# Kernel tuning notes

Measured on AMD Instinct MI355X. Metric: run time of the kernel, lower is better.

Reference implementation:

```python
import jax, jax.numpy as jnp
import numpy as np

EPS = 1e-6
H, KV, HD, FF = 16, 8, 128, 3072

def rmsnorm(x, scale):
    # qwen3_compatible: compute in fp32, scale, cast back
    xf = x.astype(jnp.float32)
    var = jnp.mean(xf * xf, axis=-1, keepdims=True)
    return ((xf * jax.lax.rsqrt(var + EPS)) * scale).astype(x.dtype)

def apply_rope(x, cos, sin):
    # x: [b, h, s, d]; cos/sin: [s, d]
    d = x.shape[-1]
    x1, x2 = x[..., : d // 2], x[..., d // 2 :]
    rotated = jnp.concatenate([-x2, x1], axis=-1)
    return (x * cos[None, None] + rotated * sin[None, None]).astype(x.dtype)

def setup_inputs() -> dict:
    key = jax.random.key(0)
    B, S, D = 2, 2048, 1024
    ks = jax.random.split(key, 8)
    x = jax.random.normal(ks[0], (B, S, D), jnp.float32)
    mask = jnp.triu(jnp.ones((S, S), dtype=bool), k=1)  # True = masked (causal)
    # Qwen3 RoPE, base 1e6, full-dim cos/sin (halves duplicated)
    pos = jnp.arange(S, dtype=jnp.float32)
    inv_freq = 1.0 / (1e6 ** (jnp.arange(0, HD, 2, dtype=jnp.float32) / HD))
    ang = pos[:, None] * inv_freq[None, :]
    cos = jnp.concatenate([jnp.cos(ang), jnp.cos(ang)], axis=-1)
    sin = jnp.concatenate([jnp.sin(ang), jnp.sin(ang)], axis=-1)
    s = 0.02
    wq = jax.random.normal(ks[1], (D, H * HD), jnp.float32) * s
    wk = jax.random.normal(ks[2], (D, KV * HD), jnp.float32) * s
    wv = jax.random.normal(ks[3], (D, KV * HD), jnp.float32) * s
    wo = jax.random.normal(ks[4], (H * HD, D), jnp.float32) * s
    fc1 = jax.random.normal(ks[5], (D, FF), jnp.float32) * s
    fc2 = jax.random.normal(ks[6], (D, FF), jnp.float32) * s
    fc3 = jax.random.normal(ks[7], (FF, D), jnp.float32) * s
    return dict(x=x, mask=mask, cos=cos, sin=sin, wq=wq, wk=wk, wv=wv, wo=wo,
                fc1=fc1, fc2=fc2, fc3=fc3,
                norm1_scale=jnp.ones((D,), jnp.float32),
                norm2_scale=jnp.ones((D,), jnp.float32),
                q_norm_scale=jnp.ones((HD,), jnp.float32),
                k_norm_scale=jnp.ones((HD,), jnp.float32))

def reference(x, mask, cos, sin, wq, wk, wv, wo, fc1, fc2, fc3,
              norm1_scale, norm2_scale, q_norm_scale, k_norm_scale):
    B, S, D = x.shape
    G = H // KV  # GQA group size
    # --- attention sublayer ---
    h = rmsnorm(x, norm1_scale)
    q = (h @ wq).reshape(B, S, H, HD).transpose(0, 2, 1, 3)   # [b,h,s,d]
    k = (h @ wk).reshape(B, S, KV, HD).transpose(0, 2, 1, 3)  # [b,kv,s,d]
    v = (h @ wv).reshape(B, S, KV, HD).transpose(0, 2, 1, 3)
    q = rmsnorm(q, q_norm_scale)
    k = rmsnorm(k, k_norm_scale)
    q = apply_rope(q, cos, sin)
    k = apply_rope(k, cos, sin)
    k = jnp.repeat(k, G, axis=1)  # repeat_interleave over head dim
    v = jnp.repeat(v, G, axis=1)
    scores = jnp.einsum('bhqd,bhkd->bhqk', q, k)
    scores = jnp.where(mask[None, None], -jnp.inf, scores)
    w = jax.nn.softmax(scores / np.float32(np.sqrt(HD)), axis=-1)
    ctx = jnp.einsum('bhqk,bhkd->bqhd', w, v).reshape(B, S, H * HD)
    x = x + ctx @ wo
    # --- SwiGLU FFN sublayer ---
    h2 = rmsnorm(x, norm2_scale)
    ff = (jax.nn.silu(h2 @ fc1) * (h2 @ fc2)) @ fc3
    return x + ff
```

## Files before the change

kernel.cpp:

```cpp
#include <hip/hip_runtime.h>

#define B_  2
#define S_  2048
#define D_  1024
#define H_  16
#define KV_ 8
#define HD_ 128
#define FF_ 3072
#define KVB 32

typedef short bf16x8 __attribute__((ext_vector_type(8)));
typedef short bf16x4 __attribute__((ext_vector_type(4)));
typedef float f32x4 __attribute__((ext_vector_type(4)));

__device__ __forceinline__ float bf2f(unsigned short u) {
    union { float f; unsigned int i; } c; c.i = ((unsigned int)u) << 16; return c.f;
}
__device__ __forceinline__ unsigned short f2bf(float f) {
    union { float f; unsigned int i; } c; c.f = f;
    unsigned int r = c.i + 0x7fffu + ((c.i >> 16) & 1u);
    return (unsigned short)(r >> 16);
}

__device__ __forceinline__ void gload_lds16(const unsigned short* g, char* ldsbase) {
    __builtin_amdgcn_global_load_lds(
        (const __attribute__((address_space(1))) unsigned int*)g,
        (__attribute__((address_space(3))) unsigned int*)ldsbase, 16, 0, 0);
}

__device__ __forceinline__ f32x4 pv_mfma(bf16x4 a, bf16x4 b, f32x4 c) {
#if __has_builtin(__builtin_amdgcn_mfma_f32_16x16x16bf16_1k)
    return __builtin_amdgcn_mfma_f32_16x16x16bf16_1k(a, b, c, 0, 0, 0);
#elif __has_builtin(__builtin_amdgcn_mfma_f32_16x16x16_bf16)
    return __builtin_amdgcn_mfma_f32_16x16x16_bf16(a, b, c, 0, 0, 0);
#else
    f32x4 d;
    asm("v_mfma_f32_16x16x16_bf16 %0, %1, %2, %3" : "=v"(d) : "v"(a), "v"(b), "v"(c));
    return d;
#endif
}

__global__ __launch_bounds__(256)
void rmsnorm_kernel(const float* __restrict__ in, const float* __restrict__ scale,
                    unsigned short* __restrict__ out) {
    const int row = blockIdx.x;
    const int t = threadIdx.x;
    const float4 v = *reinterpret_cast<const float4*>(in + (size_t)row * D_ + t * 4);
    float s = v.x * v.x + v.y * v.y + v.z * v.z + v.w * v.w;
    #pragma unroll
    for (int o = 32; o; o >>= 1) s += __shfl_down(s, o);
    __shared__ float red[4];
    const int lane = t & 63, wid = t >> 6;
    if (lane == 0) red[wid] = s;
    __syncthreads();
    s = red[0] + red[1] + red[2] + red[3];
    const float rn = rsqrtf(s * (1.0f / D_) + 1e-6f);
    const float4 sc = *reinterpret_cast<const float4*>(scale + t * 4);
    unsigned short o4[4];
    o4[0] = f2bf(v.x * rn * sc.x);
    o4[1] = f2bf(v.y * rn * sc.y);
    o4[2] = f2bf(v.z * rn * sc.z);
    o4[3] = f2bf(v.w * rn * sc.w);
    *reinterpret_cast<ushort4*>(out + (size_t)row * D_ + t * 4) =
        *reinterpret_cast<ushort4*>(o4);
}

__global__ __launch_bounds__(256)
void wtrans_kernel(const float* __restrict__ W, unsigned short* __restrict__ Wt,
                   int K, int N) {
    __shared__ float tile[32][33];
    const int t = threadIdx.x;
    const int kt = blockIdx.x * 32, nt = blockIdx.y * 32;
    {
        const int r = t >> 3, c4 = (t & 7) * 4;
        const float4 v = *reinterpret_cast<const float4*>(W + (size_t)(kt + r) * N + nt + c4);
        tile[r][c4] = v.x; tile[r][c4 + 1] = v.y; tile[r][c4 + 2] = v.z; tile[r][c4 + 3] = v.w;
    }
    __syncthreads();
    {
        const int n = t >> 3, k4 = (t & 7) * 4;
        unsigned short o[4];
        #pragma unroll
        for (int i = 0; i < 4; i++) o[i] = f2bf(tile[k4 + i][n]);
        *reinterpret_cast<ushort4*>(Wt + (size_t)(nt + n) * K + kt + k4) =
            *reinterpret_cast<ushort4*>(o);
    }
}

__global__ __launch_bounds__(512, 2)
void gemm256(const unsigned short* __restrict__ A, const unsigned short* __restrict__ Bt,
             unsigned short* __restrict__ C, int M, int N, int K, int nm) {
    __shared__ __align__(16) char lds[131072];
    const int tid = threadIdx.x;
    const int lane = tid & 63, w = tid >> 6;
    const int lm = lane & 15, lg = lane >> 4;
    const int wr = w >> 2, wc = w & 3;
    const int nwg = gridDim.x;
    const int cpx = nwg >> 3;
    const int bid = blockIdx.x;
    const int swz = (bid & 7) * cpx + (bid >> 3);
    const int m0 = (swz % nm) * 256;
    const int n0 = (swz / nm) * 256;

    f32x4 acc[8][4];
    #pragma unroll
    for (int i = 0; i < 8; ++i)
        #pragma unroll
        for (int j = 0; j < 4; ++j) acc[i][j] = (f32x4){0.f, 0.f, 0.f, 0.f};

    const int srow = tid >> 3;
    const int skel = ((tid & 7) * 8) ^ (((tid >> 5) & 1) << 4);
    const int flip = ((lm >> 2) & 1) << 5;
    const int abase = (wr * 128 + lm) * 128 + ((lg * 16) ^ flip);
    const int bbase = (wc * 64 + lm) * 128 + ((lg * 16) ^ flip);

    auto part1 = [&](int kt, int d) {
        const unsigned short* ga = A + (size_t)(m0 + srow) * K + kt * 64 + skel;
        const unsigned short* gb = Bt + (size_t)(n0 + srow) * K + kt * 64 + skel;
        char* la = lds + d * 65536 + (w << 10);
        char* lb = la + 32768;
        gload_lds16(gb,                      lb);
        gload_lds16(gb + (size_t)64 * K,     lb + 8192);
        gload_lds16(gb + (size_t)128 * K,    lb + 16384);
        gload_lds16(gb + (size_t)192 * K,    lb + 24576);
        gload_lds16(ga,                      la);
        gload_lds16(ga + (size_t)128 * K,    la + 16384);
    };
    auto part2 = [&](int kt, int d) {
        const unsigned short* ga = A + (size_t)(m0 + srow) * K + kt * 64 + skel;
        char* la = lds + d * 65536 + (w << 10);
        gload_lds16(ga + (size_t)64 * K,     la + 8192);
        gload_lds16(ga + (size_t)192 * K,    la + 24576);
    };

    part1(0, 0);
    part2(0, 0);
    asm volatile("s_waitcnt vmcnt(0)" ::: "memory");
    __builtin_amdgcn_s_barrier();

    const int ntile = K >> 6;
    for (int kt = 0; kt < ntile; ++kt) {
        const int d = kt & 1;
        const bool pf = (kt + 1 < ntile);
        const char* Ar = lds + d * 65536;
        const char* Br = Ar + 32768;
        bf16x8 bb[4][2];
        #pragma unroll
        for (int nf = 0; nf < 4; ++nf)
            #pragma unroll
            for (int s = 0; s < 2; ++s)
                bb[nf][s] = *reinterpret_cast<const bf16x8*>(Br + bbase + nf * 2048 + s * 64);
        bf16x8 aH[4][2];
        #pragma unroll
        for (int f = 0; f < 4; ++f)
            #pragma unroll
            for (int s = 0; s < 2; ++s)
                aH[f][s] = *reinterpret_cast<const bf16x8*>(Ar + abase + f * 2048 + s * 64);
        if (pf) part1(kt + 1, d ^ 1);
        __builtin_amdgcn_s_setprio(1);
        #pragma unroll
        for (int f = 0; f < 4; ++f)
            #pragma unroll
            for (int nf = 0; nf < 4; ++nf)
                #pragma unroll
                for (int s = 0; s < 2; ++s)
                    acc[f][nf] = __builtin_amdgcn_mfma_f32_16x16x32_bf16(
                        aH[f][s], bb[nf][s], acc[f][nf], 0, 0, 0);
        __builtin_amdgcn_s_setprio(0);
        if (pf) asm volatile("s_waitcnt vmcnt(6)" ::: "memory");
        else    asm volatile("s_waitcnt vmcnt(0)" ::: "memory");
        __builtin_amdgcn_s_barrier();
        #pragma unroll
        for (int f = 0; f < 4; ++f)
            #pragma unroll
            for (int s = 0; s < 2; ++s)
                aH[f][s] = *reinterpret_cast<const bf16x8*>(Ar + abase + 8192 + f * 2048 + s * 64);
        if (pf) part2(kt + 1, d ^ 1);
        __builtin_amdgcn_s_setprio(1);
        #pragma unroll
        for (int f = 0; f < 4; ++f)
            #pragma unroll
            for (int nf = 0; nf < 4; ++nf)
                #pragma unroll
                for (int s = 0; s < 2; ++s)
                    acc[4 + f][nf] = __builtin_amdgcn_mfma_f32_16x16x32_bf16(
                        aH[f][s], bb[nf][s], acc[4 + f][nf], 0, 0, 0);
        __builtin_amdgcn_s_setprio(0);
        if (pf) {
            asm volatile("s_waitcnt vmcnt(2)" ::: "memory");
            __builtin_amdgcn_s_barrier();
        }
    }

    #pragma unroll
    for (int mf = 0; mf < 8; ++mf)
        #pragma unroll
        for (int nf = 0; nf < 4; ++nf)
            #pragma unroll
            for (int r = 0; r < 4; ++r)
                C[(size_t)(m0 + wr * 128 + mf * 16 + lg * 4 + r) * N +
                  (n0 + wc * 64 + nf * 16 + lm)] = f2bf(acc[mf][nf][r]);
}

template<int EPI>
__global__ __launch_bounds__(256)
void gemm_bt(const unsigned short* __restrict__ A, const unsigned short* __restrict__ Bt,
             void* __restrict__ Cout, const float* __restrict__ resid,
             int M, int N, int K, int lda) {
    constexpr int SMB = (EPI == 2) ? 34816 : 16384;
    __shared__ __align__(16) char sm[SMB];
    const int t = threadIdx.x;
    const int lane = t & 63, w = t >> 6;
    const int m0 = blockIdx.x * 128, n0 = blockIdx.y * 128;
    const int wr = w >> 1, wc = w & 1;
    const int lm = lane & 15, lg = lane >> 4;

    f32x4 acc[4][4];
    #pragma unroll
    for (int i = 0; i < 4; i++)
        #pragma unroll
        for (int j = 0; j < 4; j++) acc[i][j] = (f32x4){0.f, 0.f, 0.f, 0.f};

    const int row0 = t >> 2, kseg = (t & 3) * 8;
    const unsigned short* Ab = A + (size_t)(m0 + row0) * lda + kseg;
    const unsigned short* Bb = Bt + (size_t)(n0 + row0) * K + kseg;
    const size_t rstepA = (size_t)64 * lda;
    const size_t rstepB = (size_t)64 * K;
    char* ldsA = sm + w * 1024;
    char* ldsB = sm + 8192 + w * 1024;

    for (int k0 = 0; k0 < K; k0 += 32) {
        gload_lds16(Ab + k0, ldsA);
        gload_lds16(Ab + rstepA + k0, ldsA + 4096);
        gload_lds16(Bb + k0, ldsB);
        gload_lds16(Bb + rstepB + k0, ldsB + 4096);
        __syncthreads();
        bf16x8 aF[4], bF[4];
        #pragma unroll
        for (int i = 0; i < 4; i++)
            aF[i] = *reinterpret_cast<const bf16x8*>(sm + (wr * 64 + i * 16 + lm) * 64 + lg * 16);
        #pragma unroll
        for (int j = 0; j < 4; j++)
            bF[j] = *reinterpret_cast<const bf16x8*>(sm + 8192 + (wc * 64 + j * 16 + lm) * 64 + lg * 16);
        #pragma unroll
        for (int i = 0; i < 4; i++)
            #pragma unroll
            for (int j = 0; j < 4; j++)
                acc[i][j] = __builtin_amdgcn_mfma_f32_16x16x32_bf16(aF[i], bF[j], acc[i][j], 0, 0, 0);
        __syncthreads();
    }

    if (EPI == 2) {
        unsigned short (*Ct)[136] = reinterpret_cast<unsigned short(*)[136]>(sm);
        #pragma unroll
        for (int i = 0; i < 4; i++)
            #pragma unroll
            for (int j = 0; j < 4; j++)
                #pragma unroll
                for (int r = 0; r < 4; r++)
                    Ct[wc * 64 + j * 16 + lm][wr * 64 + i * 16 + lg * 4 + r] = f2bf(acc[i][j][r]);
        __syncthreads();
        const int colr = t >> 1, seg = t & 1;
        unsigned short* dst = reinterpret_cast<unsigned short*>(Cout) +
                              (size_t)(n0 + colr) * M + m0 + seg * 64;
        const unsigned short* srcp = &Ct[colr][seg * 64];
        #pragma unroll
        for (int i = 0; i < 8; i++)
            reinterpret_cast<uint4*>(dst)[i] = reinterpret_cast<const uint4*>(srcp)[i];
        return;
    }

    #pragma unroll
    for (int i = 0; i < 4; i++) {
        #pragma unroll
        for (int j = 0; j < 4; j++) {
            #pragma unroll
            for (int r = 0; r < 4; r++) {
                const int row = m0 + wr * 64 + i * 16 + lg * 4 + r;
                const int col = n0 + wc * 64 + j * 16 + lm;
                const size_t idx = (size_t)row * N + col;
                if (EPI == 0) {
                    reinterpret_cast<unsigned short*>(Cout)[idx] = f2bf(acc[i][j][r]);
                } else {
                    reinterpret_cast<float*>(Cout)[idx] = resid[idx] + acc[i][j][r];
                }
            }
        }
    }
}

__global__ __launch_bounds__(128)
void qknorm_rope_kernel(unsigned short* __restrict__ qk, const float* __restrict__ scale,
                        const float* __restrict__ cosb, const float* __restrict__ sinb,
                        int ld) {
    const int row = blockIdx.x;
    const int head = blockIdx.y;
    const int s = row & (S_ - 1);
    const int t = threadIdx.x;
    unsigned short* p = qk + (size_t)row * ld + head * HD_;
    const float v = bf2f(p[t]);
    float ss = v * v;
    #pragma unroll
    for (int o = 32; o; o >>= 1) ss += __shfl_down(ss, o);
    __shared__ float red[2];
    __shared__ float vals[HD_];
    const int lane = t & 63, wid = t >> 6;
    if (lane == 0) red[wid] = ss;
    __syncthreads();
    ss = red[0] + red[1];
    const float rn = rsqrtf(ss * (1.0f / HD_) + 1e-6f);
    const float nv = v * rn * scale[t];
    vals[t] = nv;
    __syncthreads();
    const float rot = (t < 64) ? -vals[t + 64] : vals[t - 64];
    const float c = cosb[(size_t)s * HD_ + t];
    const float sn = sinb[(size_t)s * HD_ + t];
    p[t] = f2bf(nv * c + rot * sn);
}

__global__ __launch_bounds__(256)
void fattn_kernel(const unsigned short* __restrict__ qg,
                  const unsigned short* __restrict__ kg,
                  const unsigned short* __restrict__ vtg,
                  unsigned short* __restrict__ out, int qld, int kld) {
    __shared__ __align__(16) char klds[2 * 8192];
    __shared__ __align__(16) char vtlds[2 * 9216];
    const int t = threadIdx.x;
    const int lane = t & 63, w = t >> 6;
    const int lm = lane & 15, lg = lane >> 4;
    const int g = blockIdx.x;
    const int h = g & 15, b = g >> 4;
    const int qt = (int)gridDim.y - 1 - (int)blockIdx.y;
    const int kvh = h >> 1;
    const int q0b = qt * 64;
    const int q0w = q0b + w * 16;
    const float CS = 0.12752409731504826f;

    const unsigned short* qbase = qg + (size_t)(b * S_ + q0w + lm) * qld + h * HD_;
    bf16x8 qf[4];
    #pragma unroll
    for (int kk = 0; kk < 4; ++kk)
        qf[kk] = *reinterpret_cast<const bf16x8*>(qbase + kk * 32 + lg * 8);

    f32x4 acc[8];
    #pragma unroll
    for (int i = 0; i < 8; ++i) acc[i] = (f32x4){0.f, 0.f, 0.f, 0.f};
    float m = -3e38f, l = 0.f;

    const int nt = 2 * qt + 2;
    const int skv = t >> 3, sd8 = t & 7;
    const int vd = t >> 1, vseg = t & 1;
    const unsigned short* kgb = kg + (size_t)b * S_ * kld + kvh * HD_;
    const unsigned short* vgb = vtg + (size_t)(kvh * HD_) * (B_ * S_) + (size_t)b * S_;

    uint4 kr0, kr1, vr0, vr1;
    auto LOADR = [&](int kt) {
        const int kv0 = kt * KVB;
        const unsigned short* ksrc = kgb + (size_t)(kv0 + skv) * kld + sd8 * 16;
        kr0 = *reinterpret_cast<const uint4*>(ksrc);
        kr1 = *reinterpret_cast<const uint4*>(ksrc + 8);
        const unsigned short* vsrc = vgb + (size_t)vd * (B_ * S_) + kv0 + vseg * 16;
        vr0 = *reinterpret_cast<const uint4*>(vsrc);
        vr1 = *reinterpret_cast<const uint4*>(vsrc + 8);
    };
    auto WRITELDS = [&](int bufi) {
        char* kd = klds + bufi * 8192 + skv * 256;
        const int sw = (skv & 7) << 4;
        *reinterpret_cast<uint4*>(kd + ((sd8 * 32) ^ sw)) = kr0;
        *reinterpret_cast<uint4*>(kd + ((sd8 * 32 + 16) ^ sw)) = kr1;
        char* vdst = vtlds + bufi * 9216 + vd * 72 + vseg * 32;
        *reinterpret_cast<uint2*>(vdst)      = make_uint2(vr0.x, vr0.y);
        *reinterpret_cast<uint2*>(vdst + 8)  = make_uint2(vr0.z, vr0.w);
        *reinterpret_cast<uint2*>(vdst + 16) = make_uint2(vr1.x, vr1.y);
        *reinterpret_cast<uint2*>(vdst + 24) = make_uint2(vr1.z, vr1.w);
    };

    LOADR(0);
    WRITELDS(0);
    __syncthreads();

    for (int kt = 0; kt < nt; ++kt) {
        const int kv0 = kt * KVB;
        const int bufi = kt & 1;
        const bool havenext = (kt + 1 < nt);
        if (havenext) LOADR(kt + 1);
        if (kv0 <= q0w + 15) {
            f32x4 st[2];
            st[0] = (f32x4){0.f, 0.f, 0.f, 0.f};
            st[1] = (f32x4){0.f, 0.f, 0.f, 0.f};
            #pragma unroll
            for (int sub = 0; sub < 2; ++sub) {
                const int kvl = sub * 16 + lm;
                const char* krow = klds + bufi * 8192 + kvl * 256;
                const int sw = (kvl & 7) << 4;
                #pragma unroll
                for (int kk = 0; kk < 4; ++kk) {
                    const bf16x8 kf = *reinterpret_cast<const bf16x8*>(krow + ((kk * 64 + lg * 16) ^ sw));
                    st[sub] = __builtin_amdgcn_mfma_f32_16x16x32_bf16(kf, qf[kk], st[sub], 0, 0, 0);
                }
            }
            if (kv0 + KVB - 1 > q0w) {
                const int qa = q0w + lm;
                #pragma unroll
                for (int sub = 0; sub < 2; ++sub)
                    #pragma unroll
                    for (int r = 0; r < 4; ++r)
                        if (kv0 + sub * 16 + lg * 4 + r > qa) st[sub][r] = -3e38f;
            }
            float pmax = st[0][0];
            #pragma unroll
            for (int r = 1; r < 4; ++r) pmax = fmaxf(pmax, st[0][r]);
            #pragma unroll
            for (int r = 0; r < 4; ++r) pmax = fmaxf(pmax, st[1][r]);
            pmax = fmaxf(pmax, __shfl_xor(pmax, 16));
            pmax = fmaxf(pmax, __shfl_xor(pmax, 32));
            if (__any(pmax - m > 8.0f)) {
                const float mn = fmaxf(pmax, m);
                const float corr = exp2f((m - mn) * CS);
                l *= corr;
                #pragma unroll
                for (int i = 0; i < 8; ++i) acc[i] *= corr;
                m = mn;
            }
            float ps = 0.f;
            bf16x4 pb[2];
            #pragma unroll
            for (int sub = 0; sub < 2; ++sub)
                #pragma unroll
                for (int r = 0; r < 4; ++r) {
                    const float pv = exp2f((st[sub][r] - m) * CS);
                    ps += pv;
                    pb[sub][r] = (short)f2bf(pv);
                }
            ps += __shfl_xor(ps, 16);
            ps += __shfl_xor(ps, 32);
            l += ps;
            #pragma unroll
            for (int sub = 0; sub < 2; ++sub) {
                const char* vb2 = vtlds + bufi * 9216 + sub * 32 + lg * 8;
                #pragma unroll
                for (int db = 0; db < 8; ++db) {
                    const bf16x4 vf = *reinterpret_cast<const bf16x4*>(vb2 + (db * 16 + lm) * 72);
                    acc[db] = pv_mfma(vf, pb[sub], acc[db]);
                }
            }
        }
        if (havenext) WRITELDS((kt + 1) & 1);
        __syncthreads();
    }
    const float inv = 1.0f / l;
    unsigned short* ob = out + (size_t)(b * S_ + q0w + lm) * qld + h * HD_ + lg * 4;
    #pragma unroll
    for (int db = 0; db < 8; ++db) {
        unsigned short r4[4];
        #pragma unroll
        for (int r = 0; r < 4; ++r) r4[r] = f2bf(acc[db][r] * inv);
        *reinterpret_cast<uint2*>(ob + db * 16) = *reinterpret_cast<uint2*>(r4);
    }
}

__global__ __launch_bounds__(256)
void silu_mul_kernel(unsigned short* __restrict__ g, int n4) {
    const int i = blockIdx.x * 256 + threadIdx.x;
    if (i >= n4) return;
    const int r = i / (FF_ / 4);
    const int c = (i - r * (FF_ / 4)) * 4;
    const size_t off = (size_t)r * (2 * FF_) + c;
    const uint2 a = *reinterpret_cast<const uint2*>(g + off);
    const uint2 bv = *reinterpret_cast<const uint2*>(g + off + FF_);
    const unsigned int au[2] = {a.x, a.y}, bu[2] = {bv.x, bv.y};
    unsigned int rr[2];
    #pragma unroll
    for (int j = 0; j < 2; j++) {
        const float a0 = bf2f((unsigned short)(au[j] & 0xffff));
        const float a1 = bf2f((unsigned short)(au[j] >> 16));
        const float b0 = bf2f((unsigned short)(bu[j] & 0xffff));
        const float b1 = bf2f((unsigned short)(bu[j] >> 16));
        const float s0 = a0 / (1.f + __expf(-a0)) * b0;
        const float s1 = a1 / (1.f + __expf(-a1)) * b1;
        rr[j] = ((unsigned int)f2bf(s1) << 16) | (unsigned int)f2bf(s0);
    }
    *reinterpret_cast<uint2*>(g + off) = make_uint2(rr[0], rr[1]);
}

extern "C" void kernel_launch(void* const* d_in, const int* in_sizes, int n_in,
                              void* d_out, int out_size, void* d_ws, size_t ws_size,
                              hipStream_t stream) {
    const float* x    = (const float*)d_in[0];
    const float* cosb = (const float*)d_in[2];
    const float* sinb = (const float*)d_in[3];
    const float* wq   = (const float*)d_in[4];
    const float* wk   = (const float*)d_in[5];
    const float* wv   = (const float*)d_in[6];
    const float* wo   = (const float*)d_in[7];
    const float* fc1  = (const float*)d_in[8];
    const float* fc2  = (const float*)d_in[9];
    const float* fc3  = (const float*)d_in[10];
    const float* n1s  = (const float*)d_in[11];
    const float* n2s  = (const float*)d_in[12];
    const float* qns  = (const float*)d_in[13];
    const float* kns  = (const float*)d_in[14];

    char* ws = (char*)d_ws;
    const int M = B_ * S_;
    float* outf = (float*)d_out;

    unsigned short* h    = (unsigned short*)(ws);
    unsigned short* qkb  = (unsigned short*)(ws + 8388608);
    unsigned short* vtb  = (unsigned short*)(ws + 33554432);
    unsigned short* g12  = (unsigned short*)(ws + 8388608);
    float*          x2   = (float*)(ws + 58720256);
    unsigned short* wqkt = (unsigned short*)(ws + 75497472);
    unsigned short* wvt  = (unsigned short*)(ws + 81788928);
    unsigned short* wot  = (unsigned short*)(ws + 83886080);
    unsigned short* f12t = (unsigned short*)(ws + 88080384);
    unsigned short* f3t  = (unsigned short*)(ws + 100663296);
    unsigned short* wqt = wqkt;
    unsigned short* wkt = wqkt + (size_t)2048 * 1024;
    unsigned short* f1t = f12t;
    unsigned short* f2t = f12t + (size_t)3072 * 1024;

    wtrans_kernel<<<dim3(D_ / 32, (H_ * HD_) / 32), 256, 0, stream>>>(wq, wqt, D_, H_ * HD_);
    wtrans_kernel<<<dim3(D_ / 32, (KV_ * HD_) / 32), 256, 0, stream>>>(wk, wkt, D_, KV_ * HD_);
    wtrans_kernel<<<dim3(D_ / 32, (KV_ * HD_) / 32), 256, 0, stream>>>(wv, wvt, D_, KV_ * HD_);
    wtrans_kernel<<<dim3((H_ * HD_) / 32, D_ / 32), 256, 0, stream>>>(wo, wot, H_ * HD_, D_);
    wtrans_kernel<<<dim3(D_ / 32, FF_ / 32), 256, 0, stream>>>(fc1, f1t, D_, FF_);
    wtrans_kernel<<<dim3(D_ / 32, FF_ / 32), 256, 0, stream>>>(fc2, f2t, D_, FF_);
    wtrans_kernel<<<dim3(FF_ / 32, D_ / 32), 256, 0, stream>>>(fc3, f3t, FF_, D_);

    rmsnorm_kernel<<<M, 256, 0, stream>>>(x, n1s, h);
    gemm256<<<(M / 256) * (3072 / 256), 512, 0, stream>>>(h, wqkt, qkb, M, 3072, D_, M / 256);
    gemm_bt<2><<<dim3(M / 128, (KV_ * HD_) / 128), 256, 0, stream>>>(h, wvt, vtb, nullptr, M, KV_ * HD_, D_, D_);
    qknorm_rope_kernel<<<dim3(M, H_), 128, 0, stream>>>(qkb, qns, cosb, sinb, 3072);
    qknorm_rope_kernel<<<dim3(M, KV_), 128, 0, stream>>>(qkb + 2048, kns, cosb, sinb, 3072);
    fattn_kernel<<<dim3(H_ * B_, S_ / 64), 256, 0, stream>>>(qkb, qkb + 2048, vtb, qkb, 3072, 3072);
    gemm_bt<1><<<dim3(M / 128, D_ / 128), 256, 0, stream>>>(qkb, wot, x2, x, M, D_, H_ * HD_, 3072);
    rmsnorm_kernel<<<M, 256, 0, stream>>>(x2, n2s, h);
    gemm256<<<(M / 256) * (6144 / 256), 512, 0, stream>>>(h, f12t, g12, M, 6144, D_, M / 256);
    silu_mul_kernel<<<(M * FF_ / 4 + 255) / 256, 256, 0, stream>>>(g12, M * FF_ / 4);
    gemm_bt<1><<<dim3(M / 128, D_ / 128), 256, 0, stream>>>(g12, f3t, outf, x2, M, D_, FF_, 2 * FF_);
}
```

Measured before the change: 422.3 us.

## Fuse V projection into QKV GEMM and batch weight transposes into one launch

Merges the seven per-weight transpose/convert launches into a single kernel driven by a descriptor table. It also folds the V projection into the large 256-tile QKV GEMM (N=4096) and adds a separate bf16 transpose kernel that produces V^T for attention. The aim is fewer launches and better tile utilisation for V, instead of the smaller 128-tile GEMM with its LDS-transposed epilogue. The cost is an extra read and write pass over V through the new transpose kernel.

```diff
diff --git a/kernel.cpp b/kernel.cpp
--- a/kernel.cpp
+++ b/kernel.cpp
@@ -65,12 +65,28 @@
         *reinterpret_cast<ushort4*>(o4);
 }
 
+struct WTDesc {
+    const float* src[7];
+    unsigned short* dst[7];
+    int K[7];
+    int N[7];
+    int start[8];
+};
+
 __global__ __launch_bounds__(256)
-void wtrans_kernel(const float* __restrict__ W, unsigned short* __restrict__ Wt,
-                   int K, int N) {
+void wtrans_all_kernel(WTDesc d) {
     __shared__ float tile[32][33];
+    const int blk = blockIdx.x;
+    int i = 0;
+    #pragma unroll
+    for (int j = 0; j < 7; ++j) if (blk >= d.start[j + 1]) i = j + 1;
+    const int local = blk - d.start[i];
+    const int K = d.K[i], N = d.N[i];
+    const int nkt = K >> 5;
+    const int kt = (local % nkt) * 32, nt = (local / nkt) * 32;
+    const float* W = d.src[i];
+    unsigned short* Wt = d.dst[i];
     const int t = threadIdx.x;
-    const int kt = blockIdx.x * 32, nt = blockIdx.y * 32;
     {
         const int r = t >> 3, c4 = (t & 7) * 4;
         const float4 v = *reinterpret_cast<const float4*>(W + (size_t)(kt + r) * N + nt + c4);
@@ -81,8 +97,29 @@
         const int n = t >> 3, k4 = (t & 7) * 4;
         unsigned short o[4];
         #pragma unroll
-        for (int i = 0; i < 4; i++) o[i] = f2bf(tile[k4 + i][n]);
+        for (int q = 0; q < 4; q++) o[q] = f2bf(tile[k4 + q][n]);
         *reinterpret_cast<ushort4*>(Wt + (size_t)(nt + n) * K + kt + k4) =
+            *reinterpret_cast<ushort4*>(o);
+    }
+}
+
+__global__ __launch_bounds__(256)
+void vtrans_kernel(const unsigned short* __restrict__ vin, unsigned short* __restrict__ vt) {
+    __shared__ unsigned short tile[32][36];
+    const int t = threadIdx.x;
+    const int mt = blockIdx.x * 32, nt = blockIdx.y * 32;
+    {
+        const int r = t >> 3, c4 = (t & 7) * 4;
+        *reinterpret_cast<ushort4*>(&tile[r][c4]) =
+            *reinterpret_cast<const ushort4*>(vin + (size_t)(mt + r) * 4096 + nt + c4);
+    }
+    __syncthreads();
+    {
+        const int n = t >> 3, m4 = (t & 7) * 4;
+        unsigned short o[4];
+        #pragma unroll
+        for (int q = 0; q < 4; q++) o[q] = tile[m4 + q][n];
+        *reinterpret_cast<ushort4*>(vt + (size_t)(nt + n) * 4096 + mt + m4) =
             *reinterpret_cast<ushort4*>(o);
     }
 }
@@ -207,8 +244,7 @@
 void gemm_bt(const unsigned short* __restrict__ A, const unsigned short* __restrict__ Bt,
              void* __restrict__ Cout, const float* __restrict__ resid,
              int M, int N, int K, int lda) {
-    constexpr int SMB = (EPI == 2) ? 34816 : 16384;
-    __shared__ __align__(16) char sm[SMB];
+    __shared__ __align__(16) char sm[16384];
     const int t = threadIdx.x;
     const int lane = t & 63, w = t >> 6;
     const int m0 = blockIdx.x * 128, n0 = blockIdx.y * 128;
@@ -248,26 +284,6 @@
             for (int j = 0; j < 4; j++)
                 acc[i][j] = __builtin_amdgcn_mfma_f32_16x16x32_bf16(aF[i], bF[j], acc[i][j], 0, 0, 0);
         __syncthreads();
-    }
-
-    if (EPI == 2) {
-        unsigned short (*Ct)[136] = reinterpret_cast<unsigned short(*)[136]>(sm);
-        #pragma unroll
-        for (int i = 0; i < 4; i++)
-            #pragma unroll
-            for (int j = 0; j < 4; j++)
-                #pragma unroll
-                for (int r = 0; r < 4; r++)
-                    Ct[wc * 64 + j * 16 + lm][wr * 64 + i * 16 + lg * 4 + r] = f2bf(acc[i][j][r]);
-        __syncthreads();
-        const int colr = t >> 1, seg = t & 1;
-        unsigned short* dst = reinterpret_cast<unsigned short*>(Cout) +
-                              (size_t)(n0 + colr) * M + m0 + seg * 64;
-        const unsigned short* srcp = &Ct[colr][seg * 64];
-        #pragma unroll
-        for (int i = 0; i < 8; i++)
-            reinterpret_cast<uint4*>(dst)[i] = reinterpret_cast<const uint4*>(srcp)[i];
-        return;
     }
 
     #pragma unroll
@@ -505,36 +521,36 @@
     const int M = B_ * S_;
     float* outf = (float*)d_out;
 
-    unsigned short* h    = (unsigned short*)(ws);
-    unsigned short* qkb  = (unsigned short*)(ws + 8388608);
-    unsigned short* vtb  = (unsigned short*)(ws + 33554432);
-    unsigned short* g12  = (unsigned short*)(ws + 8388608);
-    float*          x2   = (float*)(ws + 58720256);
-    unsigned short* wqkt = (unsigned short*)(ws + 75497472);
-    unsigned short* wvt  = (unsigned short*)(ws + 81788928);
-    unsigned short* wot  = (unsigned short*)(ws + 83886080);
-    unsigned short* f12t = (unsigned short*)(ws + 88080384);
-    unsigned short* f3t  = (unsigned short*)(ws + 100663296);
-    unsigned short* wqt = wqkt;
-    unsigned short* wkt = wqkt + (size_t)2048 * 1024;
-    unsigned short* f1t = f12t;
-    unsigned short* f2t = f12t + (size_t)3072 * 1024;
-
-    wtrans_kernel<<<dim3(D_ / 32, (H_ * HD_) / 32), 256, 0, stream>>>(wq, wqt, D_, H_ * HD_);
-    wtrans_kernel<<<dim3(D_ / 32, (KV_ * HD_) / 32), 256, 0, stream>>>(wk, wkt, D_, KV_ * HD_);
-    wtrans_kernel<<<dim3(D_ / 32, (KV_ * HD_) / 32), 256, 0, stream>>>(wv, wvt, D_, KV_ * HD_);
-    wtrans_kernel<<<dim3((H_ * HD_) / 32, D_ / 32), 256, 0, stream>>>(wo, wot, H_ * HD_, D_);
-    wtrans_kernel<<<dim3(D_ / 32, FF_ / 32), 256, 0, stream>>>(fc1, f1t, D_, FF_);
-    wtrans_kernel<<<dim3(D_ / 32, FF_ / 32), 256, 0, stream>>>(fc2, f2t, D_, FF_);
-    wtrans_kernel<<<dim3(FF_ / 32, D_ / 32), 256, 0, stream>>>(fc3, f3t, FF_, D_);
+    unsigned short* h     = (unsigned short*)(ws);
+    unsigned short* qkvb  = (unsigned short*)(ws + 8388608);
+    unsigned short* vtb   = (unsigned short*)(ws + 41943040);
+    unsigned short* g12   = (unsigned short*)(ws + 8388608);
+    float*          x2    = (float*)(ws + 58720256);
+    unsigned short* wqkvt = (unsigned short*)(ws + 75497472);
+    unsigned short* wot   = (unsigned short*)(ws + 83886080);
+    unsigned short* f12t  = (unsigned short*)(ws + 88080384);
+    unsigned short* f3t   = (unsigned short*)(ws + 100663296);
+
+    WTDesc wd;
+    wd.src[0] = wq;  wd.dst[0] = wqkvt;                         wd.K[0] = D_;       wd.N[0] = 2048;
+    wd.src[1] = wk;  wd.dst[1] = wqkvt + (size_t)2048 * 1024;   wd.K[1] = D_;       wd.N[1] = 1024;
+    wd.src[2] = wv;  wd.dst[2] = wqkvt + (size_t)3072 * 1024;   wd.K[2] = D_;       wd.N[2] = 1024;
+    wd.src[3] = wo;  wd.dst[3] = wot;                           wd.K[3] = H_ * HD_; wd.N[3] = D_;
+    wd.src[4] = fc1; wd.dst[4] = f12t;                          wd.K[4] = D_;       wd.N[4] = FF_;
+    wd.src[5] = fc2; wd.dst[5] = f12t + (size_t)3072 * 1024;    wd.K[5] = D_;       wd.N[5] = FF_;
+    wd.src[6] = fc3; wd.dst[6] = f3t;                           wd.K[6] = FF_;      wd.N[6] = D_;
+    wd.start[0] = 0;
+    for (int i = 0; i < 7; ++i)
+        wd.start[i + 1] = wd.start[i] + (wd.K[i] / 32) * (wd.N[i] / 32);
+    wtrans_all_kernel<<<wd.start[7], 256, 0, stream>>>(wd);
 
     rmsnorm_kernel<<<M, 256, 0, stream>>>(x, n1s, h);
-    gemm256<<<(M / 256) * (3072 / 256), 512, 0, stream>>>(h, wqkt, qkb, M, 3072, D_, M / 256);
-    gemm_bt<2><<<dim3(M / 128, (KV_ * HD_) / 128), 256, 0, stream>>>(h, wvt, vtb, nullptr, M, KV_ * HD_, D_, D_);
-    qknorm_rope_kernel<<<dim3(M, H_), 128, 0, stream>>>(qkb, qns, cosb, sinb, 3072);
-    qknorm_rope_kernel<<<dim3(M, KV_), 128, 0, stream>>>(qkb + 2048, kns, cosb, sinb, 3072);
-    fattn_kernel<<<dim3(H_ * B_, S_ / 64), 256, 0, stream>>>(qkb, qkb + 2048, vtb, qkb, 3072, 3072);
-    gemm_bt<1><<<dim3(M / 128, D_ / 128), 256, 0, stream>>>(qkb, wot, x2, x, M, D_, H_ * HD_, 3072);
+    gemm256<<<(M / 256) * (4096 / 256), 512, 0, stream>>>(h, wqkvt, qkvb, M, 4096, D_, M / 256);
+    vtrans_kernel<<<dim3(M / 32, 1024 / 32), 256, 0, stream>>>(qkvb + 3072, vtb);
+    qknorm_rope_kernel<<<dim3(M, H_), 128, 0, stream>>>(qkvb, qns, cosb, sinb, 4096);
+    qknorm_rope_kernel<<<dim3(M, KV_), 128, 0, stream>>>(qkvb + 2048, kns, cosb, sinb, 4096);
+    fattn_kernel<<<dim3(H_ * B_, S_ / 64), 256, 0, stream>>>(qkvb, qkvb + 2048, vtb, qkvb, 4096, 4096);
+    gemm_bt<1><<<dim3(M / 128, D_ / 128), 256, 0, stream>>>(qkvb, wot, x2, x, M, D_, H_ * HD_, 4096);
     rmsnorm_kernel<<<M, 256, 0, stream>>>(x2, n2s, h);
     gemm256<<<(M / 256) * (6144 / 256), 512, 0, stream>>>(h, f12t, g12, M, 6144, D_, M / 256);
     silu_mul_kernel<<<(M * FF_ / 4 + 255) / 256, 256, 0, stream>>>(g12, M * FF_ / 4);
```

After: 393.8 us. 6.8% less time.
